# Performance work log

Measured on AMD Instinct MI355X. Metric: run time of the kernel, lower is better.

The kernel has to match this reference:

```python
import jax, jax.numpy as jnp
import numpy as np

EMBED_DIM = 1024
NUM_HEADS = 16
HEAD_DIM = EMBED_DIM // NUM_HEADS
ROPE_BASE = 10000.0


def _rope_cos_sin(seq_len, dim, dtype=jnp.float32):
    inv_freq = 1.0 / (ROPE_BASE ** (jnp.arange(0, dim, 2, dtype=jnp.float32) / dim))
    pos = jnp.arange(seq_len, dtype=jnp.float32)
    freqs = jnp.outer(pos, inv_freq)              # [S, dim/2]
    emb = jnp.concatenate([freqs, freqs], axis=-1)  # [S, dim]
    return jnp.cos(emb).astype(dtype), jnp.sin(emb).astype(dtype)


def _rotate_half(x):
    half = x.shape[-1] // 2
    return jnp.concatenate([-x[..., half:], x[..., :half]], axis=-1)


def setup_inputs() -> dict:
    key = jax.random.key(0)
    ks = jax.random.split(key, 12)
    B, S, E = 4, 2048, EMBED_DIM
    std = 1.0 / np.sqrt(E)
    inp = {
        'query': jax.random.normal(ks[0], (B, S, E), jnp.float32),
        'key': jax.random.normal(ks[1], (B, S, E), jnp.float32),
        'value': jax.random.normal(ks[2], (B, S, E), jnp.float32),
        'Wq': jax.random.uniform(ks[3], (E, E), jnp.float32, -std, std),
        'bq': jax.random.uniform(ks[4], (E,), jnp.float32, -std, std),
        'Wk': jax.random.uniform(ks[5], (E, E), jnp.float32, -std, std),
        'bk': jax.random.uniform(ks[6], (E,), jnp.float32, -std, std),
        'Wv': jax.random.uniform(ks[7], (E, E), jnp.float32, -std, std),
        'bv': jax.random.uniform(ks[8], (E,), jnp.float32, -std, std),
        'Wo': jax.random.uniform(ks[9], (E, E), jnp.float32, -std, std),
        'bo': jax.random.uniform(ks[10], (E,), jnp.float32, -std, std),
    }
    return inp


def reference(query, key, value, Wq, bq, Wk, bk, Wv, bv, Wo, bo):
    B, Sq, E = query.shape
    Sk = key.shape[1]
    H, D = NUM_HEADS, HEAD_DIM
    scale = D ** -0.5

    q = query @ Wq.T + bq
    k = key @ Wk.T + bk
    v = value @ Wv.T + bv

    # [B, H, S, D]
    q = q.reshape(B, Sq, H, D).transpose(0, 2, 1, 3)
    k = k.reshape(B, Sk, H, D).transpose(0, 2, 1, 3)
    v = v.reshape(B, Sk, H, D).transpose(0, 2, 1, 3)

    cos, sin = _rope_cos_sin(Sq, D, q.dtype)  # [S, D]; module slices by seq_len_q for both
    cos = cos[None, None]  # [1,1,S,D]
    sin = sin[None, None]
    q = q * cos + _rotate_half(q) * sin
    k = k * cos + _rotate_half(k) * sin

    scores = jnp.einsum('bhqd,bhkd->bhqk', q, k) * scale
    attn = jax.nn.softmax(scores, axis=-1)  # dropout p=0.0 -> identity
    out = jnp.einsum('bhqk,bhkd->bhqd', attn, v)
    out = out.transpose(0, 2, 1, 3).reshape(B, Sq, E)
    out = out @ Wo.T + bo
    attn_avg = attn.mean(axis=1)  # [B, Sq, Sk]
    return out, attn_avg
```

## Files before the change

kernel.cpp:

```cpp
#include <hip/hip_runtime.h>
#include <math.h>

#define TB 4
#define TS 2048
#define TE 1024
#define TH 16
#define TD 64
#define TM_ (TB*TS)

#define WS_Q   0
#define WS_K   8388608
#define WS_L   16777216
#define WS_TAB 16908288

typedef __attribute__((ext_vector_type(8))) short bf16x8;
typedef __attribute__((ext_vector_type(4))) float f32x4;

static __device__ inline unsigned fbits(float x) {
    union { float f; unsigned u; } v; v.f = x; return v.u;
}
static __device__ inline float bits2f(unsigned u) {
    union { unsigned u; float f; } v; v.u = u; return v.f;
}
static __device__ inline unsigned pack_rhu(float a, float b) {
    return __builtin_amdgcn_perm(fbits(b) + 0x8000u, fbits(a) + 0x8000u, 0x07060302u);
}
static __device__ inline short bf16s(float x) {
    return (short)((fbits(x) + 0x8000u) >> 16);
}
static __device__ inline void split2(float x0, float x1, unsigned& hp, unsigned& lp) {
    unsigned u0 = fbits(x0) + 0x8000u, u1 = fbits(x1) + 0x8000u;
    hp = __builtin_amdgcn_perm(u1, u0, 0x07060302u);
    float h0 = bits2f(u0 & 0xffff0000u);
    float h1 = bits2f(u1 & 0xffff0000u);
    lp = pack_rhu(x0 - h0, x1 - h1);
}

static __device__ inline void gl_lds16(const short* g, short* lds_base, int lane)
{
#if __has_builtin(__builtin_amdgcn_global_load_lds)
    __builtin_amdgcn_global_load_lds(
        (const __attribute__((address_space(1))) unsigned int*)g,
        (__attribute__((address_space(3))) unsigned int*)lds_base, 16, 0, 0);
#else
    *(uint4*)(lds_base + lane * 8) = *(const uint4*)g;
#endif
}

static __device__ inline void split_tile(const float* sp, short* dp, int key)
{
    unsigned H[16], L[16];
    #pragma unroll
    for (int c2 = 0; c2 < 8; ++c2) {
        float4 v = *(const float4*)(sp + c2 * 4);
        split2(v.x, v.y, H[2 * c2],     L[2 * c2]);
        split2(v.z, v.w, H[2 * c2 + 1], L[2 * c2 + 1]);
    }
    #pragma unroll
    for (int c = 0; c < 4; ++c) {
        *(uint4*)(dp + ((c ^ key) * 8)) =
            make_uint4(H[4 * c], H[4 * c + 1], H[4 * c + 2], H[4 * c + 3]);
        *(uint4*)(dp + (((4 + c) ^ key) * 8)) =
            make_uint4(L[4 * c], L[4 * c + 1], L[4 * c + 2], L[4 * c + 3]);
    }
}

__global__ __launch_bounds__(256, 4)
void xsplit(const float* src, short* dst)
{
    const int idx = blockIdx.x * 256 + threadIdx.x;
    const int kt = idx & 15;
    const int row = idx >> 4;
    const float* sp = src + (size_t)row * 1024 + kt * 64;
    short* dp = dst + (size_t)row * 2048 + kt * 128;
    const int key = row & 7;
    split_tile(sp,      dp,      key);
    split_tile(sp + 32, dp + 64, key);
}

__global__ __launch_bounds__(256, 4)
void wsplit(const float* __restrict__ W0, const float* __restrict__ W1,
            const float* __restrict__ W2, const float* __restrict__ W3,
            short* __restrict__ dst)
{
    const int idx = blockIdx.x * 256 + threadIdx.x;
    const int kt = idx & 15;
    const int row = idx >> 4;
    const int w = row >> 10, n = row & 1023;
    const float* Wx = (w == 0) ? W0 : (w == 1) ? W1 : (w == 2) ? W2 : W3;
    const float* sp = Wx + (size_t)n * 1024 + kt * 64;
    short* dp = dst + (size_t)row * 2048 + kt * 128;
    const int key = n & 7;
    split_tile(sp,      dp,      key);
    split_tile(sp + 32, dp + 64, key);
}

template<int MODE>
__global__ __launch_bounds__(256, 3)
void gemm_nt(const short* __restrict__ Xs, const short* __restrict__ Ws,
             const float* __restrict__ bias, float* __restrict__ out)
{
    __shared__ short A2[128 * 64];
    __shared__ short B2[128 * 64];

    const int tid  = threadIdx.x;
    const int lane = tid & 63;
    const int wv   = tid >> 6;
    const int t16  = lane & 15;
    const int quad = lane >> 4;
    const int wm   = (wv >> 1) * 64;
    const int wn   = (wv & 1) * 64;
    const int m0 = blockIdx.y * 128;
    const int n0 = blockIdx.x * 128;

    const int grow = wv * 8 + (lane >> 3);
    const int gso  = (lane & 7) * 8;
    const int cxh = ((quad) ^ (t16 & 7)) * 8;
    const int cxl = ((4 + quad) ^ (t16 & 7)) * 8;

    f32x4 acc[4][4];
    #pragma unroll
    for (int i = 0; i < 4; ++i)
        #pragma unroll
        for (int j = 0; j < 4; ++j) acc[i][j] = (f32x4){0.f, 0.f, 0.f, 0.f};

    for (int kt = 0; kt < 32; ++kt) {
        __syncthreads();
        #pragma unroll
        for (int r = 0; r < 4; ++r) {
            gl_lds16(Xs + (size_t)(m0 + r * 32 + grow) * 2048 + kt * 64 + gso,
                     &A2[(r * 32 + wv * 8) * 64], lane);
            gl_lds16(Ws + (size_t)(n0 + r * 32 + grow) * 2048 + kt * 64 + gso,
                     &B2[(r * 32 + wv * 8) * 64], lane);
        }
        __syncthreads();

        bf16x8 ah[4], al[4], bh[4], bl[4];
        #pragma unroll
        for (int i = 0; i < 4; ++i) {
            ah[i] = *(const bf16x8*)&A2[(wm + i * 16 + t16) * 64 + cxh];
            al[i] = *(const bf16x8*)&A2[(wm + i * 16 + t16) * 64 + cxl];
            bh[i] = *(const bf16x8*)&B2[(wn + i * 16 + t16) * 64 + cxh];
            bl[i] = *(const bf16x8*)&B2[(wn + i * 16 + t16) * 64 + cxl];
        }
        #pragma unroll
        for (int i = 0; i < 4; ++i)
            #pragma unroll
            for (int j = 0; j < 4; ++j) {
                acc[i][j] = __builtin_amdgcn_mfma_f32_16x16x32_bf16(ah[i], bh[j], acc[i][j], 0, 0, 0);
                acc[i][j] = __builtin_amdgcn_mfma_f32_16x16x32_bf16(al[i], bh[j], acc[i][j], 0, 0, 0);
                acc[i][j] = __builtin_amdgcn_mfma_f32_16x16x32_bf16(ah[i], bl[j], acc[i][j], 0, 0, 0);
            }
    }

    if (MODE == 2) {
        short* o16 = (short*)out;
        const int b = m0 >> 11;
        const int sbase0 = (m0 & 2047) + wm + quad * 4;
        #pragma unroll
        for (int j = 0; j < 4; ++j) {
            const int n = n0 + wn + j * 16 + t16;
            const int h = n >> 6, d = n & 63;
            const float bv = bias[n];
            const size_t base = ((size_t)(b * TH + h) * TD + d) * TS;
            #pragma unroll
            for (int i = 0; i < 4; ++i) {
                const int s = sbase0 + i * 16;
                uint2 p = make_uint2(pack_rhu(acc[i][j][0] + bv, acc[i][j][1] + bv),
                                     pack_rhu(acc[i][j][2] + bv, acc[i][j][3] + bv));
                *(uint2*)(o16 + base + s) = p;
            }
        }
        return;
    }

    #pragma unroll
    for (int j = 0; j < 4; ++j) {
        const int n = n0 + wn + j * 16 + t16;
        const float bv = bias[n];
        if (MODE == 0) {
            #pragma unroll
            for (int i = 0; i < 4; ++i)
                #pragma unroll
                for (int r = 0; r < 4; ++r) {
                    const int m = m0 + wm + i * 16 + quad * 4 + r;
                    out[(size_t)m * TE + n] = acc[i][j][r] + bv;
                }
        } else {
            const int h = n >> 6, d = n & 63;
            #pragma unroll
            for (int i = 0; i < 4; ++i)
                #pragma unroll
                for (int r = 0; r < 4; ++r) {
                    const int m = m0 + wm + i * 16 + quad * 4 + r;
                    const int bb_ = m >> 11, s = m & 2047;
                    out[((size_t)(bb_ * TH + h) * TS + s) * TD + d] = acc[i][j][r] + bv;
                }
        }
    }
}

__global__ void rope_table(float* __restrict__ tab)
{
    const int idx = blockIdx.x * 256 + threadIdx.x;
    const int d = idx & 31, s = idx >> 5;
    const float e = (float)(2 * d) / 64.0f;
    const float inv = 1.0f / powf(10000.0f, e);
    const float a = (float)s * inv;
    tab[2 * idx + 0] = cosf(a);
    tab[2 * idx + 1] = sinf(a);
}

__global__ __launch_bounds__(256, 2)
void rope_split(float* __restrict__ Q, float* __restrict__ Kv,
                const float* __restrict__ tab)
{
    const int idx = blockIdx.x * 256 + threadIdx.x;
    const int s  = idx & 2047;
    const int bh = (idx >> 11) & 63;
    const int qk = idx >> 17;
    float* P = qk ? Kv : Q;
    const float scale = qk ? 1.0f : (0.125f * 1.44269504f);
    const int key = s & 7;
    unsigned* rp = (unsigned*)(P + ((size_t)bh * TS + s) * 64);

    unsigned xu[64];
    #pragma unroll
    for (int i = 0; i < 16; ++i) {
        uint4 v = *(const uint4*)(rp + i * 4);
        xu[4 * i + 0] = v.x; xu[4 * i + 1] = v.y;
        xu[4 * i + 2] = v.z; xu[4 * i + 3] = v.w;
    }
    const float* tb = tab + (size_t)s * 64;
    #pragma unroll
    for (int d = 0; d < 32; ++d) {
        const float c = tb[2 * d], sn = tb[2 * d + 1];
        const float x0 = bits2f(xu[d]), x1 = bits2f(xu[d + 32]);
        xu[d]      = fbits((x0 * c - x1 * sn) * scale);
        xu[d + 32] = fbits((x1 * c + x0 * sn) * scale);
    }
    #pragma unroll
    for (int ch = 0; ch < 8; ++ch) {
        unsigned h[4], l[4];
        #pragma unroll
        for (int p = 0; p < 4; ++p)
            split2(bits2f(xu[ch * 8 + 2 * p]), bits2f(xu[ch * 8 + 2 * p + 1]), h[p], l[p]);
        const int slot = ch ^ key;
        *(uint4*)(rp + slot * 4)      = make_uint4(h[0], h[1], h[2], h[3]);
        *(uint4*)(rp + 32 + slot * 4) = make_uint4(l[0], l[1], l[2], l[3]);
    }
}

__global__ __launch_bounds__(512, 4)
void attn_flash(const short* __restrict__ Qs, const short* __restrict__ Ks,
                const short* __restrict__ VT, float* __restrict__ O,
                float* __restrict__ Ls)
{
    __shared__ short KhL[4096], KlL[4096];
    __shared__ short VtL[4096];
    __shared__ short PsL[8192];

    const int tid  = threadIdx.x;
    const int lane = tid & 63;
    const int wv   = tid >> 6;
    const int t16  = lane & 15;
    const int quad = lane >> 4;
    const int q0w  = wv * 16;

    const int L   = blockIdx.x + 16 * blockIdx.y + 256 * blockIdx.z;
    const int xcd = L & 7;
    const int i_  = L >> 3;
    const int qt  = i_ & 15;
    const int g   = (xcd << 3) | (i_ >> 4);
    const int h   = g & 15;
    const int b   = g >> 4;

    const int q0 = qt * 128;
    const int bh = b * TH + h;
    const short* Krb = Ks + (size_t)bh * TS * 128;
    const short* Vth = VT + (size_t)bh * TD * TS;

    const int cx0 = ((quad) ^ (t16 & 7)) * 8;
    const int cx1 = ((4 + quad) ^ (t16 & 7)) * 8;

    bf16x8 qfh[2], qfl[2];
    {
        const short* qrow = Qs + ((size_t)bh * TS + q0 + q0w + t16) * 128;
        qfh[0] = *(const bf16x8*)(qrow + cx0);
        qfh[1] = *(const bf16x8*)(qrow + cx1);
        qfl[0] = *(const bf16x8*)(qrow + 64 + cx0);
        qfl[1] = *(const bf16x8*)(qrow + 64 + cx1);
    }

    float lsum[4] = {0.f, 0.f, 0.f, 0.f};
    f32x4 o_acc[4];
    #pragma unroll
    for (int dt = 0; dt < 4; ++dt) o_acc[dt] = (f32x4){0.f, 0.f, 0.f, 0.f};

    const int krow = tid >> 3;
    const int kch  = tid & 7;
    const int ksl  = (kch ^ (krow & 7)) * 8;

    uint4 rkh = *(const uint4*)(Krb + (size_t)krow * 128 + kch * 8);
    uint4 rkl = *(const uint4*)(Krb + (size_t)krow * 128 + 64 + kch * 8);
    uint4 rvv = *(const uint4*)(Vth + (size_t)krow * TS + kch * 8);

    for (int j0 = 0; j0 < TS; j0 += 64) {
        __syncthreads();
        *(uint4*)&KhL[krow * 64 + kch * 8] = rkh;
        *(uint4*)&KlL[krow * 64 + kch * 8] = rkl;
        *(uint4*)&VtL[krow * 64 + ksl]     = rvv;
        __syncthreads();

        if (j0 + 64 < TS) {
            const short* kr = Krb + (size_t)(j0 + 64 + krow) * 128;
            rkh = *(const uint4*)(kr + kch * 8);
            rkl = *(const uint4*)(kr + 64 + kch * 8);
            rvv = *(const uint4*)(Vth + (size_t)krow * TS + j0 + 64 + kch * 8);
        }

        f32x4 sc[4];
        #pragma unroll
        for (int t = 0; t < 4; ++t) sc[t] = (f32x4){0.f, 0.f, 0.f, 0.f};
        #pragma unroll
        for (int t = 0; t < 4; ++t) {
            const int rb = (t * 16 + t16) * 64;
            bf16x8 kh0 = *(const bf16x8*)&KhL[rb + cx0];
            bf16x8 kl0 = *(const bf16x8*)&KlL[rb + cx0];
            sc[t] = __builtin_amdgcn_mfma_f32_16x16x32_bf16(qfh[0], kh0, sc[t], 0, 0, 0);
            sc[t] = __builtin_amdgcn_mfma_f32_16x16x32_bf16(qfh[0], kl0, sc[t], 0, 0, 0);
            sc[t] = __builtin_amdgcn_mfma_f32_16x16x32_bf16(qfl[0], kh0, sc[t], 0, 0, 0);
            bf16x8 kh1 = *(const bf16x8*)&KhL[rb + cx1];
            bf16x8 kl1 = *(const bf16x8*)&KlL[rb + cx1];
            sc[t] = __builtin_amdgcn_mfma_f32_16x16x32_bf16(qfh[1], kh1, sc[t], 0, 0, 0);
            sc[t] = __builtin_amdgcn_mfma_f32_16x16x32_bf16(qfh[1], kl1, sc[t], 0, 0, 0);
            sc[t] = __builtin_amdgcn_mfma_f32_16x16x32_bf16(qfl[1], kh1, sc[t], 0, 0, 0);
        }

        #pragma unroll
        for (int t = 0; t < 4; ++t) {
            float p0 = __builtin_amdgcn_exp2f(sc[t][0]);
            float p1 = __builtin_amdgcn_exp2f(sc[t][1]);
            float p2 = __builtin_amdgcn_exp2f(sc[t][2]);
            float p3 = __builtin_amdgcn_exp2f(sc[t][3]);
            lsum[0] += p0; lsum[1] += p1; lsum[2] += p2; lsum[3] += p3;
            const int cb = 2 * t + (t16 >> 3);
            const int co = t16 & 7;
            const int r0 = q0w + quad * 4;
            PsL[(r0 + 0) * 64 + ((cb ^ ((r0 + 0) & 7)) * 8) + co] = bf16s(p0);
            PsL[(r0 + 1) * 64 + ((cb ^ ((r0 + 1) & 7)) * 8) + co] = bf16s(p1);
            PsL[(r0 + 2) * 64 + ((cb ^ ((r0 + 2) & 7)) * 8) + co] = bf16s(p2);
            PsL[(r0 + 3) * 64 + ((cb ^ ((r0 + 3) & 7)) * 8) + co] = bf16s(p3);
        }

        {
            const int pr = (q0w + t16) * 64;
            bf16x8 pa0 = *(const bf16x8*)&PsL[pr + cx0];
            #pragma unroll
            for (int dt = 0; dt < 4; ++dt) {
                bf16x8 vb = *(const bf16x8*)&VtL[(dt * 16 + t16) * 64 + cx0];
                o_acc[dt] = __builtin_amdgcn_mfma_f32_16x16x32_bf16(pa0, vb, o_acc[dt], 0, 0, 0);
            }
            bf16x8 pa1 = *(const bf16x8*)&PsL[pr + cx1];
            #pragma unroll
            for (int dt = 0; dt < 4; ++dt) {
                bf16x8 vb = *(const bf16x8*)&VtL[(dt * 16 + t16) * 64 + cx1];
                o_acc[dt] = __builtin_amdgcn_mfma_f32_16x16x32_bf16(pa1, vb, o_acc[dt], 0, 0, 0);
            }
        }
    }

    #pragma unroll
    for (int r = 0; r < 4; ++r) {
        #pragma unroll
        for (int off = 1; off < 16; off <<= 1)
            lsum[r] += __shfl_xor(lsum[r], off, 16);
    }

    #pragma unroll
    for (int r = 0; r < 4; ++r) {
        const int row = q0 + q0w + quad * 4 + r;
        const float inv = 1.0f / lsum[r];
        #pragma unroll
        for (int dt = 0; dt < 4; ++dt)
            O[((size_t)(b * TS) + row) * TE + h * TD + dt * 16 + t16] = o_acc[dt][r] * inv;
        if (t16 == 0)
            Ls[(size_t)bh * TS + row] = lsum[r];
    }
}

__global__ __launch_bounds__(256, 2)
void attn_avg_k(const short* __restrict__ Qs, const short* __restrict__ Ks,
                const float* __restrict__ Ls, float* __restrict__ AV)
{
    __shared__ short Qt[128 * 64];
    __shared__ short Kt[128 * 64];
    __shared__ float ML[TH][128];

    const int tid  = threadIdx.x;
    const int lane = tid & 63;
    const int wv   = tid >> 6;
    const int t16  = lane & 15;
    const int quad = lane >> 4;
    const int wq = (wv >> 1) * 64;
    const int wj = (wv & 1) * 64;

    const int id  = blockIdx.x + 16 * blockIdx.y + 256 * blockIdx.z;
    const int xcd = id & 7;
    const int r_  = id >> 3;
    const int b   = xcd >> 1;
    const int q0  = ((xcd & 1) * 8 + (r_ >> 4)) * 128;
    const int j0  = (r_ & 15) * 128;

    #pragma unroll
    for (int i = 0; i < 8; ++i) {
        const int u = tid + 256 * i;
        const int h = u >> 7, rr = u & 127;
        ML[h][rr] = 1.0f / Ls[(size_t)(b * TH + h) * TS + q0 + rr];
    }

    const int grow = wv * 8 + (lane >> 3);
    const int gso  = (lane & 7) * 8;
    const int cxh = ((quad) ^ (t16 & 7)) * 8;
    const int cxl = ((4 + quad) ^ (t16 & 7)) * 8;

    f32x4 acc[4][4];
    #pragma unroll
    for (int mt = 0; mt < 4; ++mt)
        #pragma unroll
        for (int nt = 0; nt < 4; ++nt) acc[mt][nt] = (f32x4){0.f, 0.f, 0.f, 0.f};

    for (int h = 0; h < TH; ++h) {
        __syncthreads();
        const size_t rbq = (size_t)(b * TH + h) * TS + q0;
        const size_t rbk = (size_t)(b * TH + h) * TS + j0;
        #pragma unroll
        for (int r = 0; r < 4; ++r) {
            gl_lds16(Qs + (rbq + r * 32 + grow) * 128 + gso,
                     &Qt[(r * 32 + wv * 8) * 64], lane);
            gl_lds16(Ks + (rbk + r * 32 + grow) * 128 + gso,
                     &Kt[(r * 32 + wv * 8) * 64], lane);
        }
        __syncthreads();

        f32x4 sc[4][4];
        #pragma unroll
        for (int mt = 0; mt < 4; ++mt)
            #pragma unroll
            for (int nt = 0; nt < 4; ++nt) sc[mt][nt] = (f32x4){0.f, 0.f, 0.f, 0.f};
        #pragma unroll
        for (int ks = 0; ks < 2; ++ks) {
            const int cx = ks ? cxl : cxh;
            bf16x8 af[4], bf[4];
            #pragma unroll
            for (int mt = 0; mt < 4; ++mt)
                af[mt] = *(const bf16x8*)&Qt[(wq + mt * 16 + t16) * 64 + cx];
            #pragma unroll
            for (int nt = 0; nt < 4; ++nt)
                bf[nt] = *(const bf16x8*)&Kt[(wj + nt * 16 + t16) * 64 + cx];
            #pragma unroll
            for (int mt = 0; mt < 4; ++mt)
                #pragma unroll
                for (int nt = 0; nt < 4; ++nt)
                    sc[mt][nt] = __builtin_amdgcn_mfma_f32_16x16x32_bf16(af[mt], bf[nt], sc[mt][nt], 0, 0, 0);
        }

        #pragma unroll
        for (int mt = 0; mt < 4; ++mt) {
            const int rl = wq + mt * 16 + quad * 4;
            const float lv[4] = {ML[h][rl], ML[h][rl + 1], ML[h][rl + 2], ML[h][rl + 3]};
            #pragma unroll
            for (int nt = 0; nt < 4; ++nt)
                #pragma unroll
                for (int r = 0; r < 4; ++r)
                    acc[mt][nt][r] = fmaf(__builtin_amdgcn_exp2f(sc[mt][nt][r]), lv[r], acc[mt][nt][r]);
        }
    }

    const float inv_h = 1.0f / (float)TH;
    #pragma unroll
    for (int mt = 0; mt < 4; ++mt) {
        #pragma unroll
        for (int r = 0; r < 4; ++r) {
            const int row = q0 + wq + mt * 16 + quad * 4 + r;
            #pragma unroll
            for (int nt = 0; nt < 4; ++nt) {
                const int col = j0 + wj + nt * 16 + t16;
                AV[((size_t)b * TS + row) * TS + col] = acc[mt][nt][r] * inv_h;
            }
        }
    }
}

extern "C" void kernel_launch(void* const* d_in, const int* in_sizes, int n_in,
                              void* d_out, int out_size, void* d_ws, size_t ws_size,
                              hipStream_t stream)
{
    const float* query = (const float*)d_in[0];
    const float* key   = (const float*)d_in[1];
    const float* value = (const float*)d_in[2];
    const float* Wq = (const float*)d_in[3];
    const float* bq = (const float*)d_in[4];
    const float* Wk = (const float*)d_in[5];
    const float* bk = (const float*)d_in[6];
    const float* Wv = (const float*)d_in[7];
    const float* bv = (const float*)d_in[8];
    const float* Wo = (const float*)d_in[9];
    const float* bo = (const float*)d_in[10];

    float* ws  = (float*)d_ws;
    float* Qr  = ws + WS_Q;
    float* Kr  = ws + WS_K;
    float* Lsf = ws + WS_L;
    float* tab = ws + WS_TAB;

    float* out  = (float*)d_out;
    float* attn = out + (size_t)TB * TS * TE;
    short* VT   = (short*)attn;
    float* Ow   = attn + 4194304;
    short* Xsp  = (short*)Ow;
    short* Wsp4 = (short*)(attn + 12582912);

    dim3 blk(256);
    dim3 gproj(TE / 128, TM_ / 128);

    wsplit<<<dim3(256), blk, 0, stream>>>(Wq, Wk, Wv, Wo, Wsp4);
    rope_table<<<dim3(256), blk, 0, stream>>>(tab);

    xsplit<<<dim3(512), blk, 0, stream>>>(query, Xsp);
    gemm_nt<1><<<gproj, blk, 0, stream>>>(Xsp, Wsp4,               bq, Qr);
    xsplit<<<dim3(512), blk, 0, stream>>>(key, Xsp);
    gemm_nt<1><<<gproj, blk, 0, stream>>>(Xsp, Wsp4 + 2097152,     bk, Kr);
    xsplit<<<dim3(512), blk, 0, stream>>>(value, Xsp);
    gemm_nt<2><<<gproj, blk, 0, stream>>>(Xsp, Wsp4 + 2 * 2097152, bv, (float*)VT);

    rope_split<<<dim3(1024), blk, 0, stream>>>(Qr, Kr, tab);

    attn_flash<<<dim3(TS / 128, TH, TB), dim3(512), 0, stream>>>(
        (const short*)Qr, (const short*)Kr, VT, Ow, Lsf);

    xsplit<<<dim3(512), blk, 0, stream>>>(Ow, (short*)Ow);
    gemm_nt<0><<<gproj, blk, 0, stream>>>((const short*)Ow, Wsp4 + 3 * 2097152, bo, out);

    attn_avg_k<<<dim3(TS / 128, TS / 128, TB), blk, 0, stream>>>(
        (const short*)Qr, (const short*)Kr, Lsf, attn);
}
```

Measured before the change: 722.8 us.

## Fuse fp32-to-bf16 hi/lo split into projection GEMM with register prefetch

The separate xsplit kernels, which converted each fp32 activation matrix into a bf16 hi/lo pair in global memory, are removed. The GEMM now loads fp32 activations directly, splits them in registers and writes the swizzled tiles to LDS. It also prefetches the next k-tile into registers through plain loads instead of direct global-to-LDS copies, and remaps block indices so that neighbouring tiles share an XCD. This drops four extra kernels and their global write and read traffic, at the cost of more VGPRs and ALU work inside the GEMM main loop.

```diff
diff --git a/kernel.cpp b/kernel.cpp
--- a/kernel.cpp
+++ b/kernel.cpp
@@ -63,19 +63,6 @@
         *(uint4*)(dp + (((4 + c) ^ key) * 8)) =
             make_uint4(L[4 * c], L[4 * c + 1], L[4 * c + 2], L[4 * c + 3]);
     }
-}
-
-__global__ __launch_bounds__(256, 4)
-void xsplit(const float* src, short* dst)
-{
-    const int idx = blockIdx.x * 256 + threadIdx.x;
-    const int kt = idx & 15;
-    const int row = idx >> 4;
-    const float* sp = src + (size_t)row * 1024 + kt * 64;
-    short* dp = dst + (size_t)row * 2048 + kt * 128;
-    const int key = row & 7;
-    split_tile(sp,      dp,      key);
-    split_tile(sp + 32, dp + 64, key);
 }
 
 __global__ __launch_bounds__(256, 4)
@@ -97,7 +84,7 @@
 
 template<int MODE>
 __global__ __launch_bounds__(256, 3)
-void gemm_nt(const short* __restrict__ Xs, const short* __restrict__ Ws,
+void gemm_nt(const float* __restrict__ X, const short* __restrict__ Ws,
              const float* __restrict__ bias, float* __restrict__ out)
 {
     __shared__ short A2[128 * 64];
@@ -110,11 +97,19 @@
     const int quad = lane >> 4;
     const int wm   = (wv >> 1) * 64;
     const int wn   = (wv & 1) * 64;
-    const int m0 = blockIdx.y * 128;
-    const int n0 = blockIdx.x * 128;
-
-    const int grow = wv * 8 + (lane >> 3);
-    const int gso  = (lane & 7) * 8;
+
+    const int id  = blockIdx.x + 8 * blockIdx.y;
+    const int xcd = id & 7;
+    const int i_  = id >> 3;
+    const int m0  = (xcd * 8 + (i_ >> 3)) * 128;
+    const int n0  = (i_ & 7) * 128;
+
+    const int arow = tid >> 1;
+    const int akh  = tid & 1;
+    const int akey = arow & 7;
+    const float* Xp = X + (size_t)(m0 + arow) * 1024 + akh * 16;
+    const short* Wp = Ws + (size_t)(n0 + arow) * 2048 + akh * 32;
+
     const int cxh = ((quad) ^ (t16 & 7)) * 8;
     const int cxl = ((4 + quad) ^ (t16 & 7)) * 8;
 
@@ -124,16 +119,49 @@
         #pragma unroll
         for (int j = 0; j < 4; ++j) acc[i][j] = (f32x4){0.f, 0.f, 0.f, 0.f};
 
+    float4 ax0 = *(const float4*)(Xp);
+    float4 ax1 = *(const float4*)(Xp + 4);
+    float4 ax2 = *(const float4*)(Xp + 8);
+    float4 ax3 = *(const float4*)(Xp + 12);
+    uint4  bx0 = *(const uint4*)(Wp);
+    uint4  bx1 = *(const uint4*)(Wp + 8);
+    uint4  bx2 = *(const uint4*)(Wp + 16);
+    uint4  bx3 = *(const uint4*)(Wp + 24);
+
     for (int kt = 0; kt < 32; ++kt) {
+        unsigned H[8], L[8];
+        split2(ax0.x, ax0.y, H[0], L[0]);
+        split2(ax0.z, ax0.w, H[1], L[1]);
+        split2(ax1.x, ax1.y, H[2], L[2]);
+        split2(ax1.z, ax1.w, H[3], L[3]);
+        split2(ax2.x, ax2.y, H[4], L[4]);
+        split2(ax2.z, ax2.w, H[5], L[5]);
+        split2(ax3.x, ax3.y, H[6], L[6]);
+        split2(ax3.z, ax3.w, H[7], L[7]);
+
         __syncthreads();
-        #pragma unroll
-        for (int r = 0; r < 4; ++r) {
-            gl_lds16(Xs + (size_t)(m0 + r * 32 + grow) * 2048 + kt * 64 + gso,
-                     &A2[(r * 32 + wv * 8) * 64], lane);
-            gl_lds16(Ws + (size_t)(n0 + r * 32 + grow) * 2048 + kt * 64 + gso,
-                     &B2[(r * 32 + wv * 8) * 64], lane);
-        }
+        *(uint4*)&A2[arow * 64 + (((2 * akh + 0) ^ akey) * 8)] = make_uint4(H[0], H[1], H[2], H[3]);
+        *(uint4*)&A2[arow * 64 + (((2 * akh + 1) ^ akey) * 8)] = make_uint4(H[4], H[5], H[6], H[7]);
+        *(uint4*)&A2[arow * 64 + (((4 + 2 * akh + 0) ^ akey) * 8)] = make_uint4(L[0], L[1], L[2], L[3]);
+        *(uint4*)&A2[arow * 64 + (((4 + 2 * akh + 1) ^ akey) * 8)] = make_uint4(L[4], L[5], L[6], L[7]);
+        *(uint4*)&B2[arow * 64 + akh * 32 + 0]  = bx0;
+        *(uint4*)&B2[arow * 64 + akh * 32 + 8]  = bx1;
+        *(uint4*)&B2[arow * 64 + akh * 32 + 16] = bx2;
+        *(uint4*)&B2[arow * 64 + akh * 32 + 24] = bx3;
         __syncthreads();
+
+        if (kt + 1 < 32) {
+            const float* xp = Xp + (kt + 1) * 32;
+            ax0 = *(const float4*)(xp);
+            ax1 = *(const float4*)(xp + 4);
+            ax2 = *(const float4*)(xp + 8);
+            ax3 = *(const float4*)(xp + 12);
+            const short* wp = Wp + (kt + 1) * 64;
+            bx0 = *(const uint4*)(wp);
+            bx1 = *(const uint4*)(wp + 8);
+            bx2 = *(const uint4*)(wp + 16);
+            bx3 = *(const uint4*)(wp + 24);
+        }
 
         bf16x8 ah[4], al[4], bh[4], bl[4];
         #pragma unroll
@@ -518,7 +546,6 @@
     float* attn = out + (size_t)TB * TS * TE;
     short* VT   = (short*)attn;
     float* Ow   = attn + 4194304;
-    short* Xsp  = (short*)Ow;
     short* Wsp4 = (short*)(attn + 12582912);
 
     dim3 blk(256);
@@ -527,20 +554,16 @@
     wsplit<<<dim3(256), blk, 0, stream>>>(Wq, Wk, Wv, Wo, Wsp4);
     rope_table<<<dim3(256), blk, 0, stream>>>(tab);
 
-    xsplit<<<dim3(512), blk, 0, stream>>>(query, Xsp);
-    gemm_nt<1><<<gproj, blk, 0, stream>>>(Xsp, Wsp4,               bq, Qr);
-    xsplit<<<dim3(512), blk, 0, stream>>>(key, Xsp);
-    gemm_nt<1><<<gproj, blk, 0, stream>>>(Xsp, Wsp4 + 2097152,     bk, Kr);
-    xsplit<<<dim3(512), blk, 0, stream>>>(value, Xsp);
-    gemm_nt<2><<<gproj, blk, 0, stream>>>(Xsp, Wsp4 + 2 * 2097152, bv, (float*)VT);
+    gemm_nt<1><<<gproj, blk, 0, stream>>>(query, Wsp4,               bq, Qr);
+    gemm_nt<1><<<gproj, blk, 0, stream>>>(key,   Wsp4 + 2097152,     bk, Kr);
+    gemm_nt<2><<<gproj, blk, 0, stream>>>(value, Wsp4 + 2 * 2097152, bv, (float*)VT);
 
     rope_split<<<dim3(1024), blk, 0, stream>>>(Qr, Kr, tab);
 
     attn_flash<<<dim3(TS / 128, TH, TB), dim3(512), 0, stream>>>(
         (const short*)Qr, (const short*)Kr, VT, Ow, Lsf);
 
-    xsplit<<<dim3(512), blk, 0, stream>>>(Ow, (short*)Ow);
-    gemm_nt<0><<<gproj, blk, 0, stream>>>((const short*)Ow, Wsp4 + 3 * 2097152, bo, out);
+    gemm_nt<0><<<gproj, blk, 0, stream>>>(Ow, Wsp4 + 3 * 2097152, bo, out);
 
     attn_avg_k<<<dim3(TS / 128, TS / 128, TB), blk, 0, stream>>>(
         (const short*)Qr, (const short*)Kr, Lsf, attn);
```

After: 677.9 us. 1.07x faster.
